# Kernel optimization log

Measured on AMD Instinct MI355X. Metric: run time of the kernel, lower is better.

## Reference

```python
import jax, jax.numpy as jnp
import numpy as np

N, D, K, NUM_CLASSES = 65536, 512, 1024, 2


def setup_inputs() -> dict:
    key = jax.random.key(0)
    kx, kc = jax.random.split(key)
    x = jax.random.normal(kx, (N, D), dtype=jnp.float32)
    codebook_vectors = jax.random.normal(kc, (K, D), dtype=jnp.float32)
    codebook_classes = jnp.arange(K, dtype=jnp.int64 if jax.config.read('jax_enable_x64') else jnp.int32) % NUM_CLASSES
    return {"x": x, "codebook_vectors": codebook_vectors, "codebook_classes": codebook_classes}


def reference(x, codebook_vectors, codebook_classes):
    # Squared Euclidean distances (argmin identical to torch.cdist's p=2 argmin):
    # d2[n,k] = |x_n|^2 - 2 x_n . c_k + |c_k|^2
    x_sq = jnp.sum(x * x, axis=1, keepdims=True)            # (N, 1)
    c_sq = jnp.sum(codebook_vectors * codebook_vectors, axis=1)  # (K,)
    cross = jnp.einsum('nd,kd->nk', x, codebook_vectors)    # (N, K) GEMM
    d2 = x_sq - 2.0 * cross + c_sq[None, :]
    winners = jnp.argmin(d2, axis=1)                         # (N,)
    return codebook_classes[winners]
```

## Files before the change

kernel.cpp:

```cpp
#include <hip/hip_runtime.h>
#include <hip/hip_bf16.h>


#define N_ROWS 65536
#define DIM    512
#define K_CB   1024
#define NT     16
#define LDSBUF_F 16384
#define LDSBUF   32768

typedef short bf16x8 __attribute__((ext_vector_type(8)));
typedef float f32x4  __attribute__((ext_vector_type(4)));

__device__ __forceinline__ unsigned short f2bf_rn(float f) {
    unsigned u = __float_as_uint(f);
    unsigned r = (u + 0x7FFFu + ((u >> 16) & 1u)) >> 16;
    return (unsigned short)r;
}
__device__ __forceinline__ float bf2f(unsigned short h) {
    return __uint_as_float(((unsigned)h) << 16);
}

__device__ __forceinline__ void gload16(const void* g, void* l) {
    __builtin_amdgcn_global_load_lds(
        (const __attribute__((address_space(1))) unsigned int*)g,
        (__attribute__((address_space(3))) unsigned int*)l, 16, 0, 0);
}

__global__ void csq_kernel(const float* __restrict__ C, float* __restrict__ csq) {
    int wid  = (blockIdx.x * blockDim.x + threadIdx.x) >> 6;
    int lane = threadIdx.x & 63;
    const float4* p = (const float4*)(C + (size_t)wid * DIM);
    float4 a = p[lane * 2];
    float4 b = p[lane * 2 + 1];
    float s = a.x*a.x + a.y*a.y + a.z*a.z + a.w*a.w
            + b.x*b.x + b.y*b.y + b.z*b.z + b.w*b.w;
    #pragma unroll
    for (int m = 1; m < 64; m <<= 1) s += __shfl_xor(s, m, 64);
    if (lane == 0) csq[wid] = s;
}

__global__ void split_hi(const float* __restrict__ src,
                         unsigned short* __restrict__ h, int n4) {
    int stride = gridDim.x * 256;
    for (int i = blockIdx.x * 256 + threadIdx.x; i < n4; i += stride) {
        float4 v = ((const float4*)src)[i];
        ushort4 hh;
        hh.x = f2bf_rn(v.x); hh.y = f2bf_rn(v.y);
        hh.z = f2bf_rn(v.z); hh.w = f2bf_rn(v.w);
        ((ushort4*)h)[i] = hh;
    }
}

__global__ __launch_bounds__(512, 2)
void gemm_cross(const unsigned short* __restrict__ Xh,
                const unsigned short* __restrict__ Ch,
                _Float16* __restrict__ cross) {
    extern __shared__ unsigned short smem[];

    int b  = blockIdx.x;
    int x  = b & 7;
    int m8 = b >> 3;
    int rowtile = x * 32 + (m8 >> 2);
    int coltile = m8 & 3;
    int n0 = rowtile * 256;
    int k0 = coltile * 256;

    int tid  = threadIdx.x;
    int w    = tid >> 6;
    int lane = tid & 63;
    int wr   = w >> 2, wc = w & 3;
    int rbase = wr * 128, cbase = wc * 64;
    int lrow = lane & 15;
    int lk   = lane >> 4;
    int sg   = lk ^ ((lrow >> 1) & 3);

    int srow = tid >> 2;
    int sgrp = tid & 3;
    int r1   = (srow < 64) ? srow : srow + 64;
    int ggA  = sgrp ^ ((r1 >> 1) & 3);
    int gB   = sgrp ^ ((srow >> 1) & 3);
    size_t oA1 = (size_t)(n0 + r1) * DIM + ggA * 8;
    size_t oA2 = oA1 + (size_t)64 * DIM;
    size_t oB0 = (size_t)(k0 + srow) * DIM + gB * 8;
    size_t oB1 = oB0 + (size_t)128 * DIM;
    int rowA1_0 = (w < 4) ? w * 16 : w * 16 + 64;
    int dA1  = rowA1_0 * 32;
    int dA2  = dA1 + 2048;
    int dB0  = 8192 + w * 512;
    int dB1  = dB0 + 4096;

    f32x4 acc[8][4];
    #pragma unroll
    for (int i = 0; i < 8; i++)
        #pragma unroll
        for (int j = 0; j < 4; j++)
            acc[i][j] = (f32x4){0.f, 0.f, 0.f, 0.f};

    auto issue_tile = [&](int t) {
        unsigned short* bufn = smem + (t & 1) * LDSBUF_F;
        size_t d = (size_t)t * 32;
        gload16(Xh + oA1 + d, bufn + dA1);
        gload16(Xh + oA2 + d, bufn + dA2);
        gload16(Ch + oB0 + d, bufn + dB0);
        gload16(Ch + oB1 + d, bufn + dB1);
    };

    issue_tile(0);

    for (int t = 0; t < NT; ++t) {
        asm volatile("s_waitcnt vmcnt(0)" ::: "memory");
        __builtin_amdgcn_s_barrier();
        asm volatile("" ::: "memory");

        const unsigned short* buf = smem + (t & 1) * LDSBUF_F;
        const unsigned short* pA = buf + (rbase + lrow) * 32 + sg * 8;
        const unsigned short* pB = buf + 8192 + (cbase + lrow) * 32 + sg * 8;

        bf16x8 bh[4], ah[8];
        #pragma unroll
        for (int n = 0; n < 4; n++) bh[n] = *(const bf16x8*)(pB + n * 512);
        #pragma unroll
        for (int m = 0; m < 8; m++) ah[m] = *(const bf16x8*)(pA + m * 512);
        if (t + 1 < NT) issue_tile(t + 1);

        __builtin_amdgcn_s_setprio(1);
        #pragma unroll
        for (int m = 0; m < 8; m++)
            #pragma unroll
            for (int n = 0; n < 4; n++)
                acc[m][n] = __builtin_amdgcn_mfma_f32_16x16x32_bf16(ah[m], bh[n], acc[m][n], 0, 0, 0);
        __builtin_amdgcn_s_setprio(0);
    }

    #pragma unroll
    for (int m = 0; m < 8; m++) {
        int grow = n0 + rbase + m * 16 + lk * 4;
        #pragma unroll
        for (int r = 0; r < 4; r++) {
            _Float16* cp = cross + (size_t)(grow + r) * K_CB + k0 + cbase + lrow;
            #pragma unroll
            for (int n = 0; n < 4; n++)
                cp[n * 16] = (_Float16)acc[m][n][r];
        }
    }
}

struct H8 { _Float16 v[8]; };

__global__ __launch_bounds__(256)
void phase2_kernel(const float* __restrict__ X, const float* __restrict__ C,
                   const float* __restrict__ csq,
                   const _Float16* __restrict__ cross,
                   const int* __restrict__ classes, int* __restrict__ out) {
    int lane = threadIdx.x & 63;
    int n = blockIdx.x * 4 + (threadIdx.x >> 6);

    float cr[16];
    {
        const _Float16* cp16 = cross + (size_t)n * K_CB + lane * 16;
        H8 h0 = *(const H8*)cp16;
        H8 h1 = *(const H8*)(cp16 + 8);
        #pragma unroll
        for (int j = 0; j < 8; j++) {
            cr[j]     = (float)h0.v[j];
            cr[8 + j] = (float)h1.v[j];
        }
    }
    float q[16];
    {
        const float4* qp = (const float4*)(csq + lane * 16);
        float4 a0 = qp[0], a1 = qp[1], a2 = qp[2], a3 = qp[3];
        q[0]=a0.x;  q[1]=a0.y;  q[2]=a0.z;  q[3]=a0.w;
        q[4]=a1.x;  q[5]=a1.y;  q[6]=a1.z;  q[7]=a1.w;
        q[8]=a2.x;  q[9]=a2.y;  q[10]=a2.z; q[11]=a2.w;
        q[12]=a3.x; q[13]=a3.y; q[14]=a3.z; q[15]=a3.w;
    }

    float s[16];
    #pragma unroll
    for (int j = 0; j < 16; j++) s[j] = q[j] - 2.0f * cr[j];

    float mn = s[0];
    #pragma unroll
    for (int j = 1; j < 16; j++) mn = fminf(mn, s[j]);
    #pragma unroll
    for (int m = 1; m < 64; m <<= 1) mn = fminf(mn, __shfl_xor(mn, m, 64));

    float thr = mn + 16.0f;
    unsigned fl = 0;
    #pragma unroll
    for (int j = 0; j < 16; j++) fl |= (unsigned)(s[j] <= thr) << j;
    int cnt = __popc(fl);
    #pragma unroll
    for (int m = 1; m < 64; m <<= 1) cnt += __shfl_xor(cnt, m, 64);

    int bestk;
    if (cnt == 1) {
        int kk = 0x7fffffff;
        #pragma unroll
        for (int j = 0; j < 16; j++)
            if ((fl >> j) & 1) kk = lane * 16 + j;
        #pragma unroll
        for (int m = 1; m < 64; m <<= 1) kk = min(kk, __shfl_xor(kk, m, 64));
        bestk = kk;
    } else {
        const float4* xp = (const float4*)(X + (size_t)n * DIM + lane * 8);
        float4 x0 = xp[0], x1 = xp[1];
        float bv = 3.4e38f;
        int bk = 0x7fffffff;
        #pragma unroll 1
        for (int j = 0; j < 16; j++) {
            unsigned long long mask = __ballot((fl >> j) & 1);
            while (mask) {
                int l = __ffsll((unsigned long long)mask) - 1;
                mask &= mask - 1;
                int k = l * 16 + j;
                const float4* cp = (const float4*)(C + (size_t)k * DIM + lane * 8);
                float4 y0 = cp[0], y1 = cp[1];
                float d = x0.x*y0.x + x0.y*y0.y + x0.z*y0.z + x0.w*y0.w
                        + x1.x*y1.x + x1.y*y1.y + x1.z*y1.z + x1.w*y1.w;
                #pragma unroll
                for (int m = 1; m < 64; m <<= 1) d += __shfl_xor(d, m, 64);
                float se = csq[k] - 2.0f * d;
                if (se < bv || (se == bv && k < bk)) { bv = se; bk = k; }
            }
        }
        bestk = bk;
    }
    if (lane == 0) out[n] = classes[bestk];
}

__global__ void init_kernel(unsigned long long* __restrict__ packed) {
    int n = blockIdx.x * 256 + threadIdx.x;
    if (n < N_ROWS) packed[n] = ~0ull;
}

__global__ void split_kernel(const float* __restrict__ src,
                             unsigned short* __restrict__ h,
                             unsigned short* __restrict__ l, int n4) {
    int stride = gridDim.x * 256;
    for (int i = blockIdx.x * 256 + threadIdx.x; i < n4; i += stride) {
        float4 v = ((const float4*)src)[i];
        ushort4 hh, ll;
        float f;
        f = v.x; hh.x = f2bf_rn(f); ll.x = f2bf_rn(f - bf2f(hh.x));
        f = v.y; hh.y = f2bf_rn(f); ll.y = f2bf_rn(f - bf2f(hh.y));
        f = v.z; hh.z = f2bf_rn(f); ll.z = f2bf_rn(f - bf2f(hh.z));
        f = v.w; hh.w = f2bf_rn(f); ll.w = f2bf_rn(f - bf2f(hh.w));
        ((ushort4*)h)[i] = hh;
        ((ushort4*)l)[i] = ll;
    }
}

__global__ __launch_bounds__(512, 2)
void gemm_argmin(const unsigned short* __restrict__ Xh,
                 const unsigned short* __restrict__ Xl,
                 const unsigned short* __restrict__ Ch,
                 const unsigned short* __restrict__ Cl,
                 const float* __restrict__ csq,
                 unsigned long long* __restrict__ packed) {
    extern __shared__ unsigned short smem[];

    int b  = blockIdx.x;
    int x  = b & 7;
    int m8 = b >> 3;
    int rowtile = x * 32 + (m8 >> 2);
    int coltile = m8 & 3;
    int n0 = rowtile * 256;
    int k0 = coltile * 256;

    int tid  = threadIdx.x;
    int w    = tid >> 6;
    int lane = tid & 63;
    int wr   = w >> 2, wc = w & 3;
    int rbase = wr * 128, cbase = wc * 64;
    int lrow = lane & 15;
    int lk   = lane >> 4;
    int sg   = lk ^ ((lrow >> 1) & 3);

    int srow = tid >> 2;
    int sgrp = tid & 3;
    int r1   = (srow < 64) ? srow : srow + 64;
    int ggA  = sgrp ^ ((r1 >> 1) & 3);
    int gB   = sgrp ^ ((srow >> 1) & 3);
    size_t oA1 = (size_t)(n0 + r1) * DIM + ggA * 8;
    size_t oA2 = oA1 + (size_t)64 * DIM;
    size_t oB0 = (size_t)(k0 + srow) * DIM + gB * 8;
    size_t oB1 = oB0 + (size_t)128 * DIM;
    int rowA1_0 = (w < 4) ? w * 16 : w * 16 + 64;
    int dA1  = rowA1_0 * 32;
    int dA2  = dA1 + 2048;
    int dB0  = 16384 + w * 512;
    int dB1  = dB0 + 4096;
    int dBl0 = dB0 + 8192;
    int dBl1 = dB1 + 8192;

    f32x4 acc[8][4];
    #pragma unroll
    for (int i = 0; i < 8; i++)
        #pragma unroll
        for (int j = 0; j < 4; j++)
            acc[i][j] = (f32x4){0.f, 0.f, 0.f, 0.f};

    bf16x8 bh[4], bl[4];

    auto issue_tile = [&](int t) {
        unsigned short* bufn = smem + (t & 1) * LDSBUF;
        size_t d = (size_t)t * 32;
        gload16(Xh + oA1 + d, bufn + dA1);
        gload16(Xl + oA1 + d, bufn + 8192 + dA1);
        gload16(Ch + oB0 + d, bufn + dB0);
        gload16(Ch + oB1 + d, bufn + dB1);
        gload16(Cl + oB0 + d, bufn + dBl0);
        gload16(Cl + oB1 + d, bufn + dBl1);
        gload16(Xh + oA2 + d, bufn + dA2);
        gload16(Xl + oA2 + d, bufn + 8192 + dA2);
    };

    auto mfma_half = [&](int mb, const bf16x8* ah, const bf16x8* al) {
        __builtin_amdgcn_s_setprio(1);
        #pragma unroll
        for (int mm = 0; mm < 4; mm++)
            #pragma unroll
            for (int n = 0; n < 4; n++)
                acc[mb + mm][n] = __builtin_amdgcn_mfma_f32_16x16x32_bf16(ah[mm], bh[n], acc[mb + mm][n], 0, 0, 0);
        #pragma unroll
        for (int mm = 0; mm < 4; mm++)
            #pragma unroll
            for (int n = 0; n < 4; n++)
                acc[mb + mm][n] = __builtin_amdgcn_mfma_f32_16x16x32_bf16(ah[mm], bl[n], acc[mb + mm][n], 0, 0, 0);
        #pragma unroll
        for (int mm = 0; mm < 4; mm++)
            #pragma unroll
            for (int n = 0; n < 4; n++)
                acc[mb + mm][n] = __builtin_amdgcn_mfma_f32_16x16x32_bf16(al[mm], bh[n], acc[mb + mm][n], 0, 0, 0);
        __builtin_amdgcn_s_setprio(0);
    };

    issue_tile(0);

    for (int t = 0; t < NT; ++t) {
        asm volatile("s_waitcnt vmcnt(0)" ::: "memory");
        __builtin_amdgcn_s_barrier();
        asm volatile("" ::: "memory");

        const unsigned short* buf = smem + (t & 1) * LDSBUF;
        const unsigned short* pA = buf + (rbase + lrow) * 32 + sg * 8;
        const unsigned short* pB = buf + 16384 + (cbase + lrow) * 32 + sg * 8;

        #pragma unroll
        for (int n = 0; n < 4; n++) {
            bh[n] = *(const bf16x8*)(pB + n * 512);
            bl[n] = *(const bf16x8*)(pB + 8192 + n * 512);
        }
        bf16x8 ah[4], al[4];
        #pragma unroll
        for (int mm = 0; mm < 4; mm++) {
            ah[mm] = *(const bf16x8*)(pA + mm * 512);
            al[mm] = *(const bf16x8*)(pA + 8192 + mm * 512);
        }
        if (t + 1 < NT) issue_tile(t + 1);

        mfma_half(0, ah, al);

        bf16x8 ah2[4], al2[4];
        #pragma unroll
        for (int mm = 0; mm < 4; mm++) {
            ah2[mm] = *(const bf16x8*)(pA + (4 + mm) * 512);
            al2[mm] = *(const bf16x8*)(pA + 8192 + (4 + mm) * 512);
        }
        mfma_half(4, ah2, al2);
    }

    float cs[4];
    #pragma unroll
    for (int n = 0; n < 4; n++) cs[n] = csq[k0 + cbase + n * 16 + lrow];

    #pragma unroll
    for (int m = 0; m < 8; m++) {
        #pragma unroll
        for (int r = 0; r < 4; r++) {
            unsigned long long best = ~0ull;
            #pragma unroll
            for (int n = 0; n < 4; n++) {
                float s = cs[n] - 2.0f * acc[m][n][r];
                unsigned kb  = __float_as_uint(s);
                unsigned key = kb ^ (unsigned)(((int)kb >> 31) | 0x80000000);
                unsigned col = (unsigned)(k0 + cbase + n * 16 + lrow);
                unsigned long long pk = (((unsigned long long)key) << 32) | col;
                best = pk < best ? pk : best;
            }
            #pragma unroll
            for (int mask = 1; mask <= 8; mask <<= 1) {
                unsigned hi = __shfl_xor((unsigned)(best >> 32), mask, 64);
                unsigned lo = __shfl_xor((unsigned)(best & 0xFFFFFFFFu), mask, 64);
                unsigned long long other = (((unsigned long long)hi) << 32) | lo;
                best = other < best ? other : best;
            }
            if (lrow == 0) {
                int grow = n0 + rbase + m * 16 + lk * 4 + r;
                atomicMin(&packed[grow], best);
            }
        }
    }
}

__global__ void map_kernel(const unsigned long long* __restrict__ packed,
                           const int* __restrict__ classes,
                           int* __restrict__ out) {
    int n = blockIdx.x * 256 + threadIdx.x;
    if (n < N_ROWS) {
        unsigned col = (unsigned)(packed[n] & 0xFFFFFFFFull);
        out[n] = classes[col];
    }
}

extern "C" void kernel_launch(void* const* d_in, const int* in_sizes, int n_in,
                              void* d_out, int out_size, void* d_ws, size_t ws_size,
                              hipStream_t stream) {
    const float* X       = (const float*)d_in[0];
    const float* C       = (const float*)d_in[1];
    const int*   classes = (const int*)d_in[2];
    int*         out     = (int*)d_out;
    char* ws = (char*)d_ws;

    {
        size_t off = 0;
        float* csq = (float*)(ws + off);               off += 4096;
        unsigned short* Xh = (unsigned short*)(ws + off); off += (size_t)N_ROWS * DIM * 2;
        unsigned short* Ch = (unsigned short*)(ws + off); off += (size_t)K_CB * DIM * 2;
        _Float16* cross = (_Float16*)(ws + off);       off += (size_t)N_ROWS * K_CB * 2;
        if (ws_size >= off) {
            csq_kernel<<<K_CB / 4, 256, 0, stream>>>(C, csq);
            split_hi<<<2048, 256, 0, stream>>>(X, Xh, N_ROWS * DIM / 4);
            split_hi<<<512, 256, 0, stream>>>(C, Ch, K_CB * DIM / 4);
            hipFuncSetAttribute((const void*)gemm_cross,
                                hipFuncAttributeMaxDynamicSharedMemorySize,
                                2 * LDSBUF_F * (int)sizeof(unsigned short));
            gemm_cross<<<(N_ROWS / 256) * (K_CB / 256), 512,
                         2 * LDSBUF_F * sizeof(unsigned short), stream>>>(Xh, Ch, cross);
            phase2_kernel<<<N_ROWS / 4, 256, 0, stream>>>(X, C, csq, cross, classes, out);
            return;
        }
    }

    size_t off = 0;
    unsigned long long* packed = (unsigned long long*)(ws + off); off += (size_t)N_ROWS * 8;
    float* csq = (float*)(ws + off);                              off += (size_t)K_CB * 4;
    unsigned short* Xh = (unsigned short*)(ws + off);             off += (size_t)N_ROWS * DIM * 2;
    unsigned short* Xl = (unsigned short*)(ws + off);             off += (size_t)N_ROWS * DIM * 2;
    unsigned short* Ch = (unsigned short*)(ws + off);             off += (size_t)K_CB * DIM * 2;
    unsigned short* Cl = (unsigned short*)(ws + off);             off += (size_t)K_CB * DIM * 2;

    init_kernel<<<N_ROWS / 256, 256, 0, stream>>>(packed);
    csq_kernel<<<K_CB / 4, 256, 0, stream>>>(C, csq);
    split_kernel<<<2048, 256, 0, stream>>>(X, Xh, Xl, N_ROWS * DIM / 4);
    split_kernel<<<512, 256, 0, stream>>>(C, Ch, Cl, K_CB * DIM / 4);
    hipFuncSetAttribute((const void*)gemm_argmin,
                        hipFuncAttributeMaxDynamicSharedMemorySize,
                        2 * LDSBUF * (int)sizeof(unsigned short));
    gemm_argmin<<<(N_ROWS / 256) * (K_CB / 256), 512,
                  2 * LDSBUF * sizeof(unsigned short), stream>>>(
        Xh, Xl, Ch, Cl, csq, packed);
    map_kernel<<<N_ROWS / 256, 256, 0, stream>>>(packed, classes, out);
}
```

Before: 191.6 us.

## Fuse X bf16 conversion into GEMM A-load and fold csq into stored scores

After: 168.2 us. 1.14x faster.

```diff
diff --git a/kernel.cpp b/kernel.cpp
--- a/kernel.cpp
+++ b/kernel.cpp
@@ -19,6 +19,14 @@
 }
 __device__ __forceinline__ float bf2f(unsigned short h) {
     return __uint_as_float(((unsigned)h) << 16);
+}
+__device__ __forceinline__ bf16x8 pack_bf8(float4 a, float4 b) {
+    bf16x8 r;
+    r[0] = (short)f2bf_rn(a.x); r[1] = (short)f2bf_rn(a.y);
+    r[2] = (short)f2bf_rn(a.z); r[3] = (short)f2bf_rn(a.w);
+    r[4] = (short)f2bf_rn(b.x); r[5] = (short)f2bf_rn(b.y);
+    r[6] = (short)f2bf_rn(b.z); r[7] = (short)f2bf_rn(b.w);
+    return r;
 }
 
 __device__ __forceinline__ void gload16(const void* g, void* l) {
@@ -53,9 +61,10 @@
 }
 
 __global__ __launch_bounds__(512, 2)
-void gemm_cross(const unsigned short* __restrict__ Xh,
-                const unsigned short* __restrict__ Ch,
-                _Float16* __restrict__ cross) {
+void gemm_scores(const float* __restrict__ X,
+                 const unsigned short* __restrict__ Ch,
+                 const float* __restrict__ csq,
+                 _Float16* __restrict__ scores) {
     extern __shared__ unsigned short smem[];
 
     int b  = blockIdx.x;
@@ -75,18 +84,18 @@
     int lk   = lane >> 4;
     int sg   = lk ^ ((lrow >> 1) & 3);
 
+    int arow = tid >> 1;
+    int ag2  = (tid & 1) * 2;
+    int swA  = (arow >> 1) & 3;
+    const float* xsrc = X + (size_t)(n0 + arow) * DIM + ag2 * 8;
+    int adst0 = arow * 32 + ((ag2    ) ^ swA) * 8;
+    int adst1 = arow * 32 + ((ag2 + 1) ^ swA) * 8;
+
     int srow = tid >> 2;
     int sgrp = tid & 3;
-    int r1   = (srow < 64) ? srow : srow + 64;
-    int ggA  = sgrp ^ ((r1 >> 1) & 3);
     int gB   = sgrp ^ ((srow >> 1) & 3);
-    size_t oA1 = (size_t)(n0 + r1) * DIM + ggA * 8;
-    size_t oA2 = oA1 + (size_t)64 * DIM;
     size_t oB0 = (size_t)(k0 + srow) * DIM + gB * 8;
     size_t oB1 = oB0 + (size_t)128 * DIM;
-    int rowA1_0 = (w < 4) ? w * 16 : w * 16 + 64;
-    int dA1  = rowA1_0 * 32;
-    int dA2  = dA1 + 2048;
     int dB0  = 8192 + w * 512;
     int dB1  = dB0 + 4096;
 
@@ -97,33 +106,43 @@
         for (int j = 0; j < 4; j++)
             acc[i][j] = (f32x4){0.f, 0.f, 0.f, 0.f};
 
-    auto issue_tile = [&](int t) {
-        unsigned short* bufn = smem + (t & 1) * LDSBUF_F;
-        size_t d = (size_t)t * 32;
-        gload16(Xh + oA1 + d, bufn + dA1);
-        gload16(Xh + oA2 + d, bufn + dA2);
+    auto issue_B = [&](int tn) {
+        unsigned short* bufn = smem + (tn & 1) * LDSBUF_F;
+        size_t d = (size_t)tn * 32;
         gload16(Ch + oB0 + d, bufn + dB0);
         gload16(Ch + oB1 + d, bufn + dB1);
     };
 
-    issue_tile(0);
-
-    for (int t = 0; t < NT; ++t) {
+    float4 xa0, xa1, xa2, xa3, xb0, xb1, xb2, xb3;
+    {
+        const float4* xp = (const float4*)xsrc;
+        xa0 = xp[0]; xa1 = xp[1]; xa2 = xp[2]; xa3 = xp[3];
+    }
+    issue_B(0);
+
+    auto body = [&](int t, float4& u0, float4& u1, float4& u2, float4& u3,
+                    float4& f0, float4& f1, float4& f2, float4& f3) {
         asm volatile("s_waitcnt vmcnt(0)" ::: "memory");
+        unsigned short* abuf = smem + (t & 1) * LDSBUF_F;
+        *(bf16x8*)(abuf + adst0) = pack_bf8(u0, u1);
+        *(bf16x8*)(abuf + adst1) = pack_bf8(u2, u3);
+        asm volatile("s_waitcnt lgkmcnt(0)" ::: "memory");
         __builtin_amdgcn_s_barrier();
         asm volatile("" ::: "memory");
 
         const unsigned short* buf = smem + (t & 1) * LDSBUF_F;
         const unsigned short* pA = buf + (rbase + lrow) * 32 + sg * 8;
         const unsigned short* pB = buf + 8192 + (cbase + lrow) * 32 + sg * 8;
-
         bf16x8 bh[4], ah[8];
         #pragma unroll
         for (int n = 0; n < 4; n++) bh[n] = *(const bf16x8*)(pB + n * 512);
         #pragma unroll
         for (int m = 0; m < 8; m++) ah[m] = *(const bf16x8*)(pA + m * 512);
-        if (t + 1 < NT) issue_tile(t + 1);
-
+        if (t + 1 < NT) {
+            const float4* xp = (const float4*)(xsrc + (t + 1) * 32);
+            f0 = xp[0]; f1 = xp[1]; f2 = xp[2]; f3 = xp[3];
+            issue_B(t + 1);
+        }
         __builtin_amdgcn_s_setprio(1);
         #pragma unroll
         for (int m = 0; m < 8; m++)
@@ -131,17 +150,26 @@
             for (int n = 0; n < 4; n++)
                 acc[m][n] = __builtin_amdgcn_mfma_f32_16x16x32_bf16(ah[m], bh[n], acc[m][n], 0, 0, 0);
         __builtin_amdgcn_s_setprio(0);
-    }
+    };
+
+    for (int tt = 0; tt < NT; tt += 2) {
+        body(tt,     xa0, xa1, xa2, xa3, xb0, xb1, xb2, xb3);
+        body(tt + 1, xb0, xb1, xb2, xb3, xa0, xa1, xa2, xa3);
+    }
+
+    float cs[4];
+    #pragma unroll
+    for (int n = 0; n < 4; n++) cs[n] = csq[k0 + cbase + n * 16 + lrow];
 
     #pragma unroll
     for (int m = 0; m < 8; m++) {
         int grow = n0 + rbase + m * 16 + lk * 4;
         #pragma unroll
         for (int r = 0; r < 4; r++) {
-            _Float16* cp = cross + (size_t)(grow + r) * K_CB + k0 + cbase + lrow;
+            _Float16* sp = scores + (size_t)(grow + r) * K_CB + k0 + cbase + lrow;
             #pragma unroll
             for (int n = 0; n < 4; n++)
-                cp[n * 16] = (_Float16)acc[m][n][r];
+                sp[n * 16] = (_Float16)(cs[n] - 2.0f * acc[m][n][r]);
         }
     }
 }
@@ -151,35 +179,22 @@
 __global__ __launch_bounds__(256)
 void phase2_kernel(const float* __restrict__ X, const float* __restrict__ C,
                    const float* __restrict__ csq,
-                   const _Float16* __restrict__ cross,
+                   const _Float16* __restrict__ scores,
                    const int* __restrict__ classes, int* __restrict__ out) {
     int lane = threadIdx.x & 63;
     int n = blockIdx.x * 4 + (threadIdx.x >> 6);
 
-    float cr[16];
+    float s[16];
     {
-        const _Float16* cp16 = cross + (size_t)n * K_CB + lane * 16;
-        H8 h0 = *(const H8*)cp16;
-        H8 h1 = *(const H8*)(cp16 + 8);
+        const _Float16* sp16 = scores + (size_t)n * K_CB + lane * 16;
+        H8 h0 = *(const H8*)sp16;
+        H8 h1 = *(const H8*)(sp16 + 8);
         #pragma unroll
         for (int j = 0; j < 8; j++) {
-            cr[j]     = (float)h0.v[j];
-            cr[8 + j] = (float)h1.v[j];
-        }
-    }
-    float q[16];
-    {
-        const float4* qp = (const float4*)(csq + lane * 16);
-        float4 a0 = qp[0], a1 = qp[1], a2 = qp[2], a3 = qp[3];
-        q[0]=a0.x;  q[1]=a0.y;  q[2]=a0.z;  q[3]=a0.w;
-        q[4]=a1.x;  q[5]=a1.y;  q[6]=a1.z;  q[7]=a1.w;
-        q[8]=a2.x;  q[9]=a2.y;  q[10]=a2.z; q[11]=a2.w;
-        q[12]=a3.x; q[13]=a3.y; q[14]=a3.z; q[15]=a3.w;
-    }
-
-    float s[16];
-    #pragma unroll
-    for (int j = 0; j < 16; j++) s[j] = q[j] - 2.0f * cr[j];
+            s[j]     = (float)h0.v[j];
+            s[8 + j] = (float)h1.v[j];
+        }
+    }
 
     float mn = s[0];
     #pragma unroll
@@ -427,20 +442,19 @@
 
     {
         size_t off = 0;
-        float* csq = (float*)(ws + off);               off += 4096;
-        unsigned short* Xh = (unsigned short*)(ws + off); off += (size_t)N_ROWS * DIM * 2;
+        float* csq = (float*)(ws + off);                  off += 4096;
         unsigned short* Ch = (unsigned short*)(ws + off); off += (size_t)K_CB * DIM * 2;
-        _Float16* cross = (_Float16*)(ws + off);       off += (size_t)N_ROWS * K_CB * 2;
+        _Float16* scores = (_Float16*)(ws + off);         off += (size_t)N_ROWS * K_CB * 2;
         if (ws_size >= off) {
             csq_kernel<<<K_CB / 4, 256, 0, stream>>>(C, csq);
-            split_hi<<<2048, 256, 0, stream>>>(X, Xh, N_ROWS * DIM / 4);
             split_hi<<<512, 256, 0, stream>>>(C, Ch, K_CB * DIM / 4);
-            hipFuncSetAttribute((const void*)gemm_cross,
+            hipFuncSetAttribute((const void*)gemm_scores,
                                 hipFuncAttributeMaxDynamicSharedMemorySize,
                                 2 * LDSBUF_F * (int)sizeof(unsigned short));
-            gemm_cross<<<(N_ROWS / 256) * (K_CB / 256), 512,
-                         2 * LDSBUF_F * sizeof(unsigned short), stream>>>(Xh, Ch, cross);
-            phase2_kernel<<<N_ROWS / 4, 256, 0, stream>>>(X, C, csq, cross, classes, out);
+            gemm_scores<<<(N_ROWS / 256) * (K_CB / 256), 512,
+                          2 * LDSBUF_F * sizeof(unsigned short), stream>>>(
+                X, Ch, csq, scores);
+            phase2_kernel<<<N_ROWS / 4, 256, 0, stream>>>(X, C, csq, scores, classes, out);
             return;
         }
     }
```
